# Optimization experiments

Hardware: AMD Instinct MI355X
Metric: run time of the kernel (lower is better)

Reference implementation:

```python
import jax, jax.numpy as jnp
import numpy as np

BITS = 8
BOUND = 2.0 ** (BITS - 1) - 1.0  # 127, symmetric int8 bound
EPS = 1e-6


def fake_quant(x, scale):
    """Symmetric fake quantization with straight-through estimator."""
    q = jnp.clip(jnp.round(x * scale), -BOUND, BOUND) / scale
    return x + jax.lax.stop_gradient(q - x)


def dense_aqt(x, w, b, mask):
    """AQT-style quantized dense: per-tensor input scale (masked stats),
    per-output-channel weight scale, int8-range fake quant, float GEMM.
    x: [N, Cin], w: [Cin, Cout], b: [Cout], mask: [N, 1]."""
    x_max = jnp.max(jnp.abs(x * mask))                       # masked per-tensor stat
    sx = BOUND / jnp.maximum(x_max, EPS)
    w_max = jnp.max(jnp.abs(w), axis=0, keepdims=True)        # [1, Cout]
    sw = BOUND / jnp.maximum(w_max, EPS)
    xq = fake_quant(x, sx)
    wq = fake_quant(w, sw)
    return jnp.matmul(xq, wq) + b


def setup_inputs() -> dict:
    key = jax.random.key(0)
    k1, k2, k3 = jax.random.split(key, 3)
    B, S, C, H = 4, 2048, 1024, 4096
    inputs = jax.random.normal(k1, (B, S, C), dtype=jnp.float32)
    padding_mask = jnp.ones((B, S, 1), dtype=jnp.float32)
    W1 = jax.random.normal(k2, (C, H), dtype=jnp.float32) * (1.0 / np.sqrt(C))
    b1 = jnp.zeros((H,), dtype=jnp.float32)
    W2 = jax.random.normal(k3, (H, C), dtype=jnp.float32) * (1.0 / np.sqrt(H))
    b2 = jnp.zeros((C,), dtype=jnp.float32)
    return {"inputs": inputs, "padding_mask": padding_mask,
            "W1": W1, "b1": b1, "W2": W2, "b2": b2}


def reference(inputs, padding_mask, W1, b1, W2, b2):
    B, S, C = inputs.shape
    x = inputs.reshape(B * S, C)
    m = padding_mask.reshape(B * S, 1)
    h = jax.nn.relu(dense_aqt(x, W1, b1, m))   # dropout is no-op (deterministic)
    out = dense_aqt(h, W2, b2, m)              # dropout is no-op (deterministic)
    return out.reshape(B, S, C)
```

## Files before the change

kernel.cpp:

```cpp
#include <hip/hip_runtime.h>
#include <hip/hip_fp16.h>
#include <stdint.h>


#define EPSQ 1e-6f
typedef int v4i __attribute__((ext_vector_type(4)));
typedef int v16i __attribute__((ext_vector_type(16)));

__device__ __forceinline__ void async16(const int8_t* g, int8_t* l) {
  __builtin_amdgcn_global_load_lds(
      (const __attribute__((address_space(1))) void*)g,
      (__attribute__((address_space(3))) void*)l, 16, 0, 0);
}
__device__ __forceinline__ unsigned short f2h(float f) {
  __half h = __float2half(f);
  return *(unsigned short*)&h;
}
__device__ __forceinline__ float4 max4(float4 m, float4 v) {
  m.x = fmaxf(m.x, fabsf(v.x)); m.y = fmaxf(m.y, fabsf(v.y));
  m.z = fmaxf(m.z, fabsf(v.z)); m.w = fmaxf(m.w, fabsf(v.w));
  return m;
}
__device__ __forceinline__ unsigned qmb(float x, float s) {
  return __float_as_uint(fmaf(x, s, 12582912.0f)) & 0xffu;
}
__device__ __forceinline__ unsigned q4f(float4 f, float s) {
  return qmb(f.x, s) | (qmb(f.y, s) << 8) | (qmb(f.z, s) << 16) |
         (__float_as_uint(fmaf(f.w, s, 12582912.0f)) << 24);
}
__device__ __forceinline__ unsigned q4h(unsigned ua, unsigned ub,
                                        __half2 s2, __half2 m2) {
  __half2 ha = __hfma2(*(__half2*)&ua, s2, m2);
  __half2 hb = __hfma2(*(__half2*)&ub, s2, m2);
  unsigned va = *(unsigned*)&ha, vb = *(unsigned*)&hb;
#if __has_builtin(__builtin_amdgcn_perm)
  return __builtin_amdgcn_perm(vb, va, 0x06040200u);
#else
  return (va & 0xffu) | ((va >> 8) & 0xff00u) |
         ((vb & 0xffu) << 16) | (((vb >> 8) & 0xff00u) << 16);
#endif
}

__global__ __launch_bounds__(256) void k_stats(
    const float* __restrict__ x, const float* __restrict__ mask,
    const float* __restrict__ W1, const float* __restrict__ W2,
    float* __restrict__ pmaxX, float* __restrict__ pcm1, float* __restrict__ pcm2) {
  const int bx = blockIdx.x, tid = threadIdx.x;
  if (bx < 64) {
    const int sp = bx & 15, cg = bx >> 4;
    const int col = cg * 1024 + tid * 4;
    float4 m = {0.f, 0.f, 0.f, 0.f};
#pragma unroll 8
    for (int r = 0; r < 64; ++r)
      m = max4(m, *(const float4*)(W1 + (size_t)(sp * 64 + r) * 4096 + col));
    *(float4*)(pcm1 + sp * 4096 + col) = m;
  } else if (bx < 128) {
    const int sp = bx - 64;
    const int col = tid * 4;
    float4 m = {0.f, 0.f, 0.f, 0.f};
#pragma unroll 8
    for (int r = 0; r < 64; ++r)
      m = max4(m, *(const float4*)(W2 + (size_t)(sp * 64 + r) * 1024 + col));
    *(float4*)(pcm2 + sp * 1024 + col) = m;
  } else {
    __shared__ float red[4];
    const int b = bx - 128;
    float lmax = 0.f;
    for (int c = b * 256 + tid; c < 1048576; c += 262144) {
      size_t idx = (size_t)c * 8;
      float mk = fabsf(mask[idx >> 10]);
      float4 m4 = {0.f, 0.f, 0.f, 0.f};
      m4 = max4(m4, *(const float4*)(x + idx));
      m4 = max4(m4, *(const float4*)(x + idx + 4));
      lmax = fmaxf(lmax, fmaxf(fmaxf(m4.x, m4.y), fmaxf(m4.z, m4.w)) * mk);
    }
    for (int s = 32; s; s >>= 1) lmax = fmaxf(lmax, __shfl_down(lmax, s));
    if ((tid & 63) == 0) red[tid >> 6] = lmax;
    __syncthreads();
    if (tid == 0)
      pmaxX[b] = fmaxf(fmaxf(red[0], red[1]), fmaxf(red[2], red[3]));
  }
}

__global__ __launch_bounds__(256) void k_quant(
    const float* __restrict__ x, const float* __restrict__ W1, const float* __restrict__ W2,
    const float* __restrict__ pmaxX, const float* __restrict__ pcm1, const float* __restrict__ pcm2,
    int8_t* __restrict__ qx, int8_t* __restrict__ qw1, int8_t* __restrict__ qw2,
    float* __restrict__ cm1, float* __restrict__ cm2, float* __restrict__ scG) {
  const int bx = blockIdx.x, tid = threadIdx.x;
  if (bx < 2048) {
    __shared__ float red[4];
    float v = fmaxf(fmaxf(pmaxX[tid], pmaxX[tid + 256]),
                    fmaxf(pmaxX[tid + 512], pmaxX[tid + 768]));
    for (int s = 32; s; s >>= 1) v = fmaxf(v, __shfl_down(v, s));
    if ((tid & 63) == 0) red[tid >> 6] = v;
    __syncthreads();
    const float xmax = fmaxf(fmaxf(red[0], red[1]), fmaxf(red[2], red[3]));
    if (bx == 0 && tid == 0) scG[0] = xmax;
    const float s = 127.0f / fmaxf(xmax, EPSQ);
    const int wave = tid >> 6, lane = tid & 63;
    const int f = bx * 4 + wave;
    const int r = (f >> 5) * 32 + (lane & 31);
    const int k = (f & 31) * 32 + (lane >> 5) * 16;
    const float4* src = (const float4*)(x + (size_t)r * 1024 + k);
    uint4 o;
    o.x = q4f(src[0], s); o.y = q4f(src[1], s);
    o.z = q4f(src[2], s); o.w = q4f(src[3], s);
    *(uint4*)(qx + (size_t)f * 1024 + lane * 16) = o;
  } else if (bx < 2304) {
    int id = (bx - 2048) * 256 + tid;
    int n4 = id & 1023, kc = id >> 10;
    const int col = n4 * 4;
    float4 cm = {0.f, 0.f, 0.f, 0.f};
#pragma unroll
    for (int sp = 0; sp < 16; ++sp) {
      float4 p = *(const float4*)(pcm1 + sp * 4096 + col);
      cm.x = fmaxf(cm.x, p.x); cm.y = fmaxf(cm.y, p.y);
      cm.z = fmaxf(cm.z, p.z); cm.w = fmaxf(cm.w, p.w);
    }
    if (kc == 0) *(float4*)(cm1 + col) = cm;
    const float s0 = 127.0f / fmaxf(cm.x, EPSQ), s1 = 127.0f / fmaxf(cm.y, EPSQ);
    const float s2 = 127.0f / fmaxf(cm.z, EPSQ), s3 = 127.0f / fmaxf(cm.w, EPSQ);
    union { int8_t p[16]; uint4 v; } u0, u1, u2, u3;
#pragma unroll
    for (int j = 0; j < 16; ++j) {
      float4 f = *(const float4*)(W1 + (size_t)(kc * 16 + j) * 4096 + col);
      u0.p[j] = (int8_t)qmb(f.x, s0); u1.p[j] = (int8_t)qmb(f.y, s1);
      u2.p[j] = (int8_t)qmb(f.z, s2); u3.p[j] = (int8_t)qmb(f.w, s3);
    }
    int8_t* base = qw1 + ((size_t)(col >> 5) * 32 + (kc >> 1)) * 1024 +
                   (kc & 1) * 512 + (col & 31) * 16;
    *(uint4*)(base) = u0.v;      *(uint4*)(base + 16) = u1.v;
    *(uint4*)(base + 32) = u2.v; *(uint4*)(base + 48) = u3.v;
  } else {
    int id = (bx - 2304) * 256 + tid;
    int n4 = id & 255, kc = id >> 8;
    const int col = n4 * 4;
    float4 cm = {0.f, 0.f, 0.f, 0.f};
#pragma unroll
    for (int sp = 0; sp < 64; ++sp) {
      float4 p = *(const float4*)(pcm2 + sp * 1024 + col);
      cm.x = fmaxf(cm.x, p.x); cm.y = fmaxf(cm.y, p.y);
      cm.z = fmaxf(cm.z, p.z); cm.w = fmaxf(cm.w, p.w);
    }
    if (kc == 0) *(float4*)(cm2 + col) = cm;
    const float s0 = 127.0f / fmaxf(cm.x, EPSQ), s1 = 127.0f / fmaxf(cm.y, EPSQ);
    const float s2 = 127.0f / fmaxf(cm.z, EPSQ), s3 = 127.0f / fmaxf(cm.w, EPSQ);
    union { int8_t p[16]; uint4 v; } u0, u1, u2, u3;
#pragma unroll
    for (int j = 0; j < 16; ++j) {
      float4 f = *(const float4*)(W2 + (size_t)(kc * 16 + j) * 1024 + col);
      u0.p[j] = (int8_t)qmb(f.x, s0); u1.p[j] = (int8_t)qmb(f.y, s1);
      u2.p[j] = (int8_t)qmb(f.z, s2); u3.p[j] = (int8_t)qmb(f.w, s3);
    }
    int8_t* base = qw2 + ((size_t)(col >> 5) * 128 + (kc >> 1)) * 1024 +
                   (kc & 1) * 512 + (col & 31) * 16;
    *(uint4*)(base) = u0.v;      *(uint4*)(base + 16) = u1.v;
    *(uint4*)(base + 32) = u2.v; *(uint4*)(base + 48) = u3.v;
  }
}

__global__ __launch_bounds__(256, 5) void gemm1(
    const int8_t* __restrict__ A, const int8_t* __restrict__ Bt,
    const float* __restrict__ sxp, const float* __restrict__ cmax,
    const float* __restrict__ bias, const float* __restrict__ mask,
    unsigned short* __restrict__ hfrag, float* __restrict__ pmaxH) {
  constexpr int KF = 2, Kf = 32;
  __shared__ __align__(16) int8_t lsA[2][KF * 4096];
  __shared__ __align__(16) int8_t lsB[2][KF * 4096];
  __shared__ float red[4];
  const int tid = threadIdx.x;
  const int wave = tid >> 6, lane = tid & 63;
  const int m0 = blockIdx.x * 128, n0 = blockIdx.y * 128;
  const int wm = (wave & 1) * 64, wn = (wave >> 1) * 64;

  v16i acc[2][2] = {};

  const int8_t* gA[KF]; const int8_t* gB[KF];
  int8_t* dA[KF]; int8_t* dB[KF];
#pragma unroll
  for (int kc = 0; kc < KF; ++kc) {
    gA[kc] = A + ((size_t)((m0 >> 5) + wave) * Kf + kc) * 1024 + lane * 16;
    gB[kc] = Bt + ((size_t)((n0 >> 5) + wave) * Kf + kc) * 1024 + lane * 16;
    dA[kc] = lsA[0] + (kc * 4 + wave) * 1024 + lane * 16;
    dB[kc] = lsB[0] + (kc * 4 + wave) * 1024 + lane * 16;
  }

  const int nsteps = 1024 / (32 * KF);
#pragma unroll
  for (int kc = 0; kc < KF; ++kc) { async16(gA[kc], dA[kc]); async16(gB[kc], dB[kc]); }

  const int mI = (wave & 1) * 2, nI = (wave >> 1) * 2;

  for (int kb = 0; kb < nsteps; ++kb) {
    const int cur = kb & 1;
    const int co = cur * (KF * 4096);
    __syncthreads();
    if (kb + 1 < nsteps) {
      const size_t ko = (size_t)(kb + 1) * (KF * 1024);
      const int po = (cur ^ 1) * (KF * 4096);
#pragma unroll
      for (int kc = 0; kc < KF; ++kc) {
        async16(gA[kc] + ko, dA[kc] + po);
        async16(gB[kc] + ko, dB[kc] + po);
      }
    }
#pragma unroll
    for (int kc = 0; kc < KF; ++kc) {
      v4i af[2], bf[2];
#pragma unroll
      for (int mt = 0; mt < 2; ++mt)
        af[mt] = *(const v4i*)(lsA[0] + co + (kc * 4 + mI + mt) * 1024 + lane * 16);
#pragma unroll
      for (int nt = 0; nt < 2; ++nt)
        bf[nt] = *(const v4i*)(lsB[0] + co + (kc * 4 + nI + nt) * 1024 + lane * 16);
#pragma unroll
      for (int mt = 0; mt < 2; ++mt)
#pragma unroll
        for (int nt = 0; nt < 2; ++nt)
          acc[mt][nt] = __builtin_amdgcn_mfma_i32_32x32x32_i8(af[mt], bf[nt], acc[mt][nt], 0, 0, 0);
    }
  }

  const float asc = fmaxf(sxp[0], EPSQ) * (1.0f / 127.0f);
  const int cl = lane & 31;
  const int rbase = 4 * (lane >> 5);

  float bsc[2], bv[2];
#pragma unroll
  for (int nt = 0; nt < 2; ++nt) {
    int col = n0 + wn + nt * 32 + cl;
    bsc[nt] = fmaxf(cmax[col], EPSQ) * (1.0f / 127.0f) * asc;
    bv[nt] = bias[col];
  }

  const int hwoff = (cl >> 4) * 512 + (cl & 15);
  float lmax = 0.f;
#pragma unroll
  for (int mt = 0; mt < 2; ++mt) {
    const size_t rowblk = (size_t)((m0 + wm) >> 5) + mt;
#pragma unroll
    for (int g = 0; g < 4; ++g)
#pragma unroll
      for (int r2 = 0; r2 < 4; ++r2) {
        const int rloc = g * 8 + r2 + rbase;
        const int row = m0 + wm + mt * 32 + rloc;
        const float mk = fabsf(mask[row]);
#pragma unroll
        for (int nt = 0; nt < 2; ++nt) {
          const size_t kblk = (size_t)((n0 + wn) >> 5) + nt;
          float v = (float)acc[mt][nt][g * 4 + r2] * bsc[nt] + bv[nt];
          v = fmaxf(v, 0.f);
          hfrag[(rowblk * 128 + kblk) * 1024 + hwoff + rloc * 16] = f2h(v);
          lmax = fmaxf(lmax, v * mk);
        }
      }
  }
  for (int s = 32; s; s >>= 1) lmax = fmaxf(lmax, __shfl_down(lmax, s));
  if (lane == 0) red[wave] = lmax;
  __syncthreads();
  if (tid == 0)
    pmaxH[blockIdx.x * gridDim.y + blockIdx.y] =
        fmaxf(fmaxf(red[0], red[1]), fmaxf(red[2], red[3]));
}

__global__ __launch_bounds__(256, 2) void gemm2(
    const unsigned short* __restrict__ hfrag, const int8_t* __restrict__ Bt,
    const float* __restrict__ pmaxH, const float* __restrict__ cmax,
    const float* __restrict__ bias, float* __restrict__ out) {
  constexpr int KF = 4, Kf = 128;
  __shared__ __align__(16) int8_t lsA[2][KF * 4096];
  __shared__ __align__(16) int8_t lsB[2][KF * 4096];
  __shared__ float red[4];
  const int tid = threadIdx.x;
  const int wave = tid >> 6, lane = tid & 63;

  float v = 0.f;
#pragma unroll
  for (int j = 0; j < 8; ++j) v = fmaxf(v, pmaxH[tid + 256 * j]);
  for (int s = 32; s; s >>= 1) v = fmaxf(v, __shfl_down(v, s));
  if (lane == 0) red[wave] = v;
  __syncthreads();
  const float hmax = fmaxf(fmaxf(red[0], red[1]), fmaxf(red[2], red[3]));
  const float asc = fmaxf(hmax, EPSQ) * (1.0f / 127.0f);
  const __half sh = __float2half_rn(127.0f / fmaxf(hmax, EPSQ));
  const __half2 s2 = __halves2half2(sh, sh);
  const __half mh = __float2half_rn(1536.0f);
  const __half2 m2 = __halves2half2(mh, mh);

  const int m0 = blockIdx.x * 128, n0 = blockIdx.y * 128;
  const int wm = (wave & 1) * 64, wn = (wave >> 1) * 64;

  v16i acc[2][2] = {};

  const uint4* hA = (const uint4*)hfrag;
  size_t aIdx[KF]; const int8_t* gB[KF]; int8_t* dA[KF]; int8_t* dB[KF];
#pragma unroll
  for (int kc = 0; kc < KF; ++kc) {
    aIdx[kc] = ((size_t)((m0 >> 5) + wave) * Kf + kc) * 128 + lane * 2;
    gB[kc] = Bt + ((size_t)((n0 >> 5) + wave) * Kf + kc) * 1024 + lane * 16;
    dA[kc] = lsA[0] + (kc * 4 + wave) * 1024 + lane * 16;
    dB[kc] = lsB[0] + (kc * 4 + wave) * 1024 + lane * 16;
  }

  const int nsteps = 4096 / (32 * KF);
#pragma unroll
  for (int kc = 0; kc < KF; ++kc) {
    uint4 a = hA[aIdx[kc]], b = hA[aIdx[kc] + 1];
    uint4 o;
    o.x = q4h(a.x, a.y, s2, m2); o.y = q4h(a.z, a.w, s2, m2);
    o.z = q4h(b.x, b.y, s2, m2); o.w = q4h(b.z, b.w, s2, m2);
    *(uint4*)dA[kc] = o;
    async16(gB[kc], dB[kc]);
  }

  const int mI = (wave & 1) * 2, nI = (wave >> 1) * 2;

  for (int kb = 0; kb < nsteps; ++kb) {
    const int cur = kb & 1;
    const int co = cur * (KF * 4096);
    __syncthreads();
    uint4 pa[KF], pb[KF];
    const bool more = (kb + 1 < nsteps);
    const int po = (cur ^ 1) * (KF * 4096);
    if (more) {
#pragma unroll
      for (int kc = 0; kc < KF; ++kc) {
        const size_t ai = aIdx[kc] + (size_t)(kb + 1) * (KF * 128);
        pa[kc] = hA[ai];
        pb[kc] = hA[ai + 1];
        async16(gB[kc] + (size_t)(kb + 1) * (KF * 1024), dB[kc] + po);
      }
    }
#pragma unroll
    for (int kc = 0; kc < KF; ++kc) {
      v4i af[2], bf[2];
#pragma unroll
      for (int mt = 0; mt < 2; ++mt)
        af[mt] = *(const v4i*)(lsA[0] + co + (kc * 4 + mI + mt) * 1024 + lane * 16);
#pragma unroll
      for (int nt = 0; nt < 2; ++nt)
        bf[nt] = *(const v4i*)(lsB[0] + co + (kc * 4 + nI + nt) * 1024 + lane * 16);
#pragma unroll
      for (int mt = 0; mt < 2; ++mt)
#pragma unroll
        for (int nt = 0; nt < 2; ++nt)
          acc[mt][nt] = __builtin_amdgcn_mfma_i32_32x32x32_i8(af[mt], bf[nt], acc[mt][nt], 0, 0, 0);
    }
    if (more) {
#pragma unroll
      for (int kc = 0; kc < KF; ++kc) {
        uint4 o;
        o.x = q4h(pa[kc].x, pa[kc].y, s2, m2); o.y = q4h(pa[kc].z, pa[kc].w, s2, m2);
        o.z = q4h(pb[kc].x, pb[kc].y, s2, m2); o.w = q4h(pb[kc].z, pb[kc].w, s2, m2);
        *(uint4*)(dA[kc] + po) = o;
      }
    }
  }

  const int cl = lane & 31;
  const int rbase = 4 * (lane >> 5);
  float bsc[2], bv[2];
#pragma unroll
  for (int nt = 0; nt < 2; ++nt) {
    int col = n0 + wn + nt * 32 + cl;
    bsc[nt] = fmaxf(cmax[col], EPSQ) * (1.0f / 127.0f) * asc;
    bv[nt] = bias[col];
  }
#pragma unroll
  for (int mt = 0; mt < 2; ++mt)
#pragma unroll
    for (int g = 0; g < 4; ++g)
#pragma unroll
      for (int r2 = 0; r2 < 4; ++r2) {
        int row = m0 + wm + mt * 32 + g * 8 + r2 + rbase;
        float* orow = out + (size_t)row * 1024 + n0 + wn + cl;
#pragma unroll
        for (int nt = 0; nt < 2; ++nt)
          orow[nt * 32] = (float)acc[mt][nt][g * 4 + r2] * bsc[nt] + bv[nt];
      }
}

extern "C" void kernel_launch(void* const* d_in, const int* in_sizes, int n_in,
                              void* d_out, int out_size, void* d_ws, size_t ws_size,
                              hipStream_t stream) {
  const float* x  = (const float*)d_in[0];
  const float* mk = (const float*)d_in[1];
  const float* W1 = (const float*)d_in[2];
  const float* b1 = (const float*)d_in[3];
  const float* W2 = (const float*)d_in[4];
  const float* b2 = (const float*)d_in[5];
  float* out = (float*)d_out;

  float* scG   = (float*)d_ws;
  float* pmaxX = scG + 8;
  float* pmaxH = pmaxX + 1024;
  float* pcm1  = pmaxH + 2048;
  float* pcm2  = pcm1 + 65536;
  float* cm1   = pcm2 + 65536;
  float* cm2   = cm1 + 4096;
  int8_t* qx  = (int8_t*)(cm2 + 1024);
  int8_t* qw1 = qx  + (size_t)8192 * 1024;
  int8_t* qw2 = qw1 + (size_t)4096 * 1024;
  unsigned short* h = (unsigned short*)(qw2 + (size_t)1024 * 4096);

  k_stats<<<1152, 256, 0, stream>>>(x, mk, W1, W2, pmaxX, pcm1, pcm2);
  k_quant<<<2560, 256, 0, stream>>>(x, W1, W2, pmaxX, pcm1, pcm2,
                                    qx, qw1, qw2, cm1, cm2, scG);
  gemm1<<<dim3(64, 32), 256, 0, stream>>>(qx, qw1, scG, cm1, b1, mk, h, pmaxH);
  gemm2<<<dim3(64, 8), 256, 0, stream>>>(h, qw2, pmaxH, cm2, b2, out);
}
```

Measured before the change: 237.1 us.

## Stage gemm1 output through swizzled LDS; restructure gemm2 to 8 waves with deeper prefetch

gemm1 now writes its fp16 h fragments into a bank-swizzled LDS tile and then copies them to global memory as coalesced 16-byte stores, replacing scattered 2-byte global writes. gemm2 moves to 512-thread blocks with 8 waves, each computing a 64x32 sub-tile with K-fragment 2. It prefetches the A operand two steps ahead in registers and uses explicit waitcnt/barrier control. It also remaps blocks to XCDs so each XCD handles contiguous M rows for L2 reuse. The risks are more register pressure, extra LDS sync in the gemm1 epilogue, and hand-written waitcnt counts that may be fragile.

```diff
diff --git a/kernel.cpp b/kernel.cpp
--- a/kernel.cpp
+++ b/kernel.cpp
@@ -39,6 +39,9 @@
   return (va & 0xffu) | ((va >> 8) & 0xff00u) |
          ((vb & 0xffu) << 16) | (((vb >> 8) & 0xff00u) << 16);
 #endif
+}
+__device__ __forceinline__ int swzh(int b) {
+  return b ^ (((b >> 10) & 1) << 5) ^ (((b >> 7) & 1) << 6);
 }
 
 __global__ __launch_bounds__(256) void k_stats(
@@ -166,9 +169,9 @@
     const float* __restrict__ bias, const float* __restrict__ mask,
     unsigned short* __restrict__ hfrag, float* __restrict__ pmaxH) {
   constexpr int KF = 2, Kf = 32;
-  __shared__ __align__(16) int8_t lsA[2][KF * 4096];
-  __shared__ __align__(16) int8_t lsB[2][KF * 4096];
-  __shared__ float red[4];
+  __shared__ __align__(16) int8_t smem[32768];
+  int8_t* const lsA = smem;
+  int8_t* const lsB = smem + 16384;
   const int tid = threadIdx.x;
   const int wave = tid >> 6, lane = tid & 63;
   const int m0 = blockIdx.x * 128, n0 = blockIdx.y * 128;
@@ -182,8 +185,8 @@
   for (int kc = 0; kc < KF; ++kc) {
     gA[kc] = A + ((size_t)((m0 >> 5) + wave) * Kf + kc) * 1024 + lane * 16;
     gB[kc] = Bt + ((size_t)((n0 >> 5) + wave) * Kf + kc) * 1024 + lane * 16;
-    dA[kc] = lsA[0] + (kc * 4 + wave) * 1024 + lane * 16;
-    dB[kc] = lsB[0] + (kc * 4 + wave) * 1024 + lane * 16;
+    dA[kc] = lsA + (kc * 4 + wave) * 1024 + lane * 16;
+    dB[kc] = lsB + (kc * 4 + wave) * 1024 + lane * 16;
   }
 
   const int nsteps = 1024 / (32 * KF);
@@ -210,10 +213,10 @@
       v4i af[2], bf[2];
 #pragma unroll
       for (int mt = 0; mt < 2; ++mt)
-        af[mt] = *(const v4i*)(lsA[0] + co + (kc * 4 + mI + mt) * 1024 + lane * 16);
+        af[mt] = *(const v4i*)(lsA + co + (kc * 4 + mI + mt) * 1024 + lane * 16);
 #pragma unroll
       for (int nt = 0; nt < 2; ++nt)
-        bf[nt] = *(const v4i*)(lsB[0] + co + (kc * 4 + nI + nt) * 1024 + lane * 16);
+        bf[nt] = *(const v4i*)(lsB + co + (kc * 4 + nI + nt) * 1024 + lane * 16);
 #pragma unroll
       for (int mt = 0; mt < 2; ++mt)
 #pragma unroll
@@ -234,150 +237,164 @@
     bv[nt] = bias[col];
   }
 
-  const int hwoff = (cl >> 4) * 512 + (cl & 15);
+  const int hwb = ((cl >> 4) * 512 + (cl & 15)) * 2;
   float lmax = 0.f;
+  __syncthreads();
 #pragma unroll
   for (int mt = 0; mt < 2; ++mt) {
-    const size_t rowblk = (size_t)((m0 + wm) >> 5) + mt;
+    const int rbl = (wm >> 5) + mt;
 #pragma unroll
     for (int g = 0; g < 4; ++g)
 #pragma unroll
       for (int r2 = 0; r2 < 4; ++r2) {
         const int rloc = g * 8 + r2 + rbase;
-        const int row = m0 + wm + mt * 32 + rloc;
-        const float mk = fabsf(mask[row]);
+        const float mk = fabsf(mask[m0 + wm + mt * 32 + rloc]);
 #pragma unroll
         for (int nt = 0; nt < 2; ++nt) {
-          const size_t kblk = (size_t)((n0 + wn) >> 5) + nt;
+          const int kbl = (wn >> 5) + nt;
           float v = (float)acc[mt][nt][g * 4 + r2] * bsc[nt] + bv[nt];
           v = fmaxf(v, 0.f);
-          hfrag[(rowblk * 128 + kblk) * 1024 + hwoff + rloc * 16] = f2h(v);
+          *(unsigned short*)(smem + swzh((rbl * 4 + kbl) * 2048 + hwb + rloc * 32)) = f2h(v);
           lmax = fmaxf(lmax, v * mk);
         }
       }
   }
   for (int s = 32; s; s >>= 1) lmax = fmaxf(lmax, __shfl_down(lmax, s));
-  if (lane == 0) red[wave] = lmax;
+  __syncthreads();
+  const size_t gfb = (size_t)(m0 >> 5) * 128 + (n0 >> 5);
+#pragma unroll
+  for (int i = 0; i < 8; ++i) {
+    const int o = i * 4096 + tid * 16;
+    uint4 vv = *(const uint4*)(smem + swzh(o));
+    const int f = o >> 11;
+    *(uint4*)((int8_t*)hfrag +
+              (gfb + (size_t)(f >> 2) * 128 + (f & 3)) * 2048 + (o & 2047)) = vv;
+  }
+  __syncthreads();
+  float* redf = (float*)smem;
+  if (lane == 0) redf[wave] = lmax;
   __syncthreads();
   if (tid == 0)
     pmaxH[blockIdx.x * gridDim.y + blockIdx.y] =
-        fmaxf(fmaxf(red[0], red[1]), fmaxf(red[2], red[3]));
-}
-
-__global__ __launch_bounds__(256, 2) void gemm2(
+        fmaxf(fmaxf(redf[0], redf[1]), fmaxf(redf[2], redf[3]));
+}
+
+__global__ __launch_bounds__(512, 4) void gemm2(
     const unsigned short* __restrict__ hfrag, const int8_t* __restrict__ Bt,
     const float* __restrict__ pmaxH, const float* __restrict__ cmax,
     const float* __restrict__ bias, float* __restrict__ out) {
-  constexpr int KF = 4, Kf = 128;
-  __shared__ __align__(16) int8_t lsA[2][KF * 4096];
-  __shared__ __align__(16) int8_t lsB[2][KF * 4096];
-  __shared__ float red[4];
+  constexpr int KF = 2, Kf = 128;
+  __shared__ __align__(16) int8_t smem[32768];
+  int8_t* const lsA = smem;
+  int8_t* const lsB = smem + 16384;
   const int tid = threadIdx.x;
   const int wave = tid >> 6, lane = tid & 63;
 
+  float* red = (float*)smem;
   float v = 0.f;
 #pragma unroll
-  for (int j = 0; j < 8; ++j) v = fmaxf(v, pmaxH[tid + 256 * j]);
+  for (int j = 0; j < 4; ++j) v = fmaxf(v, pmaxH[tid + 512 * j]);
   for (int s = 32; s; s >>= 1) v = fmaxf(v, __shfl_down(v, s));
   if (lane == 0) red[wave] = v;
   __syncthreads();
-  const float hmax = fmaxf(fmaxf(red[0], red[1]), fmaxf(red[2], red[3]));
+  float hmax = red[0];
+#pragma unroll
+  for (int j = 1; j < 8; ++j) hmax = fmaxf(hmax, red[j]);
+  __syncthreads();
   const float asc = fmaxf(hmax, EPSQ) * (1.0f / 127.0f);
   const __half sh = __float2half_rn(127.0f / fmaxf(hmax, EPSQ));
   const __half2 s2 = __halves2half2(sh, sh);
   const __half mh = __float2half_rn(1536.0f);
   const __half2 m2 = __halves2half2(mh, mh);
 
-  const int m0 = blockIdx.x * 128, n0 = blockIdx.y * 128;
-  const int wm = (wave & 1) * 64, wn = (wave >> 1) * 64;
-
-  v16i acc[2][2] = {};
-
+  const int bid = blockIdx.x;
+  const int xcd = bid & 7, slot = bid >> 3;
+  const int m0 = ((xcd << 3) + (slot >> 3)) * 128;
+  const int n0 = (slot & 7) * 128;
+  const int wm = (wave & 1) * 64, wn = (wave >> 1) * 32;
+
+  v16i acc[2] = {};
+
+  const int skc = wave >> 2, sfr = wave & 3;
   const uint4* hA = (const uint4*)hfrag;
-  size_t aIdx[KF]; const int8_t* gB[KF]; int8_t* dA[KF]; int8_t* dB[KF];
-#pragma unroll
-  for (int kc = 0; kc < KF; ++kc) {
-    aIdx[kc] = ((size_t)((m0 >> 5) + wave) * Kf + kc) * 128 + lane * 2;
-    gB[kc] = Bt + ((size_t)((n0 >> 5) + wave) * Kf + kc) * 1024 + lane * 16;
-    dA[kc] = lsA[0] + (kc * 4 + wave) * 1024 + lane * 16;
-    dB[kc] = lsB[0] + (kc * 4 + wave) * 1024 + lane * 16;
-  }
+  const size_t aIdx = ((size_t)((m0 >> 5) + sfr) * Kf + skc) * 128 + lane * 2;
+  const int8_t* gB = Bt + ((size_t)((n0 >> 5) + sfr) * Kf + skc) * 1024 + lane * 16;
+  int8_t* const dA = lsA + (skc * 4 + sfr) * 1024 + lane * 16;
+  int8_t* const dB = lsB + (skc * 4 + sfr) * 1024 + lane * 16;
 
   const int nsteps = 4096 / (32 * KF);
-#pragma unroll
-  for (int kc = 0; kc < KF; ++kc) {
-    uint4 a = hA[aIdx[kc]], b = hA[aIdx[kc] + 1];
+  const int mI = (wave & 1) * 2, nb = wave >> 1;
+
+  uint4 rA0 = {0, 0, 0, 0}, rB0 = {0, 0, 0, 0};
+  uint4 rA1 = {0, 0, 0, 0}, rB1 = {0, 0, 0, 0};
+
+  {
+    uint4 a = hA[aIdx], b = hA[aIdx + 1];
+    async16(gB, dB);
+    __builtin_amdgcn_sched_barrier(0);
+    rA1 = hA[aIdx + (size_t)(KF * 128)];
+    rB1 = hA[aIdx + (size_t)(KF * 128) + 1];
     uint4 o;
     o.x = q4h(a.x, a.y, s2, m2); o.y = q4h(a.z, a.w, s2, m2);
     o.z = q4h(b.x, b.y, s2, m2); o.w = q4h(b.z, b.w, s2, m2);
-    *(uint4*)dA[kc] = o;
-    async16(gB[kc], dB[kc]);
-  }
-
-  const int mI = (wave & 1) * 2, nI = (wave >> 1) * 2;
-
+    *(uint4*)dA = o;
+  }
+  asm volatile("s_waitcnt lgkmcnt(0)" ::: "memory");
+  asm volatile("s_waitcnt vmcnt(2)" ::: "memory");
+  __builtin_amdgcn_s_barrier();
+  __builtin_amdgcn_sched_barrier(0);
+
+#pragma unroll 2
   for (int kb = 0; kb < nsteps; ++kb) {
     const int cur = kb & 1;
-    const int co = cur * (KF * 4096);
-    __syncthreads();
-    uint4 pa[KF], pb[KF];
+    const int co = cur * 8192, po = co ^ 8192;
     const bool more = (kb + 1 < nsteps);
-    const int po = (cur ^ 1) * (KF * 4096);
+    const bool deep = (kb + 2 < nsteps);
     if (more) {
-#pragma unroll
-      for (int kc = 0; kc < KF; ++kc) {
-        const size_t ai = aIdx[kc] + (size_t)(kb + 1) * (KF * 128);
-        pa[kc] = hA[ai];
-        pb[kc] = hA[ai + 1];
-        async16(gB[kc] + (size_t)(kb + 1) * (KF * 1024), dB[kc] + po);
+      async16(gB + (size_t)(kb + 1) * (KF * 1024), dB + po);
+      __builtin_amdgcn_sched_barrier(0);
+      if (deep) {
+        const size_t ai = aIdx + (size_t)(kb + 2) * (KF * 128);
+        if (cur) { rA1 = hA[ai]; rB1 = hA[ai + 1]; }
+        else     { rA0 = hA[ai]; rB0 = hA[ai + 1]; }
       }
     }
 #pragma unroll
     for (int kc = 0; kc < KF; ++kc) {
-      v4i af[2], bf[2];
-#pragma unroll
-      for (int mt = 0; mt < 2; ++mt)
-        af[mt] = *(const v4i*)(lsA[0] + co + (kc * 4 + mI + mt) * 1024 + lane * 16);
-#pragma unroll
-      for (int nt = 0; nt < 2; ++nt)
-        bf[nt] = *(const v4i*)(lsB[0] + co + (kc * 4 + nI + nt) * 1024 + lane * 16);
-#pragma unroll
-      for (int mt = 0; mt < 2; ++mt)
-#pragma unroll
-        for (int nt = 0; nt < 2; ++nt)
-          acc[mt][nt] = __builtin_amdgcn_mfma_i32_32x32x32_i8(af[mt], bf[nt], acc[mt][nt], 0, 0, 0);
+      v4i af0 = *(const v4i*)(lsA + co + (kc * 4 + mI) * 1024 + lane * 16);
+      v4i af1 = *(const v4i*)(lsA + co + (kc * 4 + mI + 1) * 1024 + lane * 16);
+      v4i bf  = *(const v4i*)(lsB + co + (kc * 4 + nb) * 1024 + lane * 16);
+      acc[0] = __builtin_amdgcn_mfma_i32_32x32x32_i8(af0, bf, acc[0], 0, 0, 0);
+      acc[1] = __builtin_amdgcn_mfma_i32_32x32x32_i8(af1, bf, acc[1], 0, 0, 0);
     }
     if (more) {
-#pragma unroll
-      for (int kc = 0; kc < KF; ++kc) {
-        uint4 o;
-        o.x = q4h(pa[kc].x, pa[kc].y, s2, m2); o.y = q4h(pa[kc].z, pa[kc].w, s2, m2);
-        o.z = q4h(pb[kc].x, pb[kc].y, s2, m2); o.w = q4h(pb[kc].z, pb[kc].w, s2, m2);
-        *(uint4*)(dA[kc] + po) = o;
-      }
+      const uint4 pa = cur ? rA0 : rA1;
+      const uint4 pb = cur ? rB0 : rB1;
+      uint4 o;
+      o.x = q4h(pa.x, pa.y, s2, m2); o.y = q4h(pa.z, pa.w, s2, m2);
+      o.z = q4h(pb.x, pb.y, s2, m2); o.w = q4h(pb.z, pb.w, s2, m2);
+      *(uint4*)(dA + po) = o;
+      asm volatile("s_waitcnt lgkmcnt(0)" ::: "memory");
+      if (deep) asm volatile("s_waitcnt vmcnt(2)" ::: "memory");
+      else      asm volatile("s_waitcnt vmcnt(0)" ::: "memory");
+      __builtin_amdgcn_s_barrier();
+      __builtin_amdgcn_sched_barrier(0);
     }
   }
 
   const int cl = lane & 31;
   const int rbase = 4 * (lane >> 5);
-  float bsc[2], bv[2];
-#pragma unroll
-  for (int nt = 0; nt < 2; ++nt) {
-    int col = n0 + wn + nt * 32 + cl;
-    bsc[nt] = fmaxf(cmax[col], EPSQ) * (1.0f / 127.0f) * asc;
-    bv[nt] = bias[col];
-  }
+  const int col = n0 + wn + cl;
+  const float bsc = fmaxf(cmax[col], EPSQ) * (1.0f / 127.0f) * asc;
+  const float bv = bias[col];
 #pragma unroll
   for (int mt = 0; mt < 2; ++mt)
 #pragma unroll
     for (int g = 0; g < 4; ++g)
 #pragma unroll
       for (int r2 = 0; r2 < 4; ++r2) {
-        int row = m0 + wm + mt * 32 + g * 8 + r2 + rbase;
-        float* orow = out + (size_t)row * 1024 + n0 + wn + cl;
-#pragma unroll
-        for (int nt = 0; nt < 2; ++nt)
-          orow[nt * 32] = (float)acc[mt][nt][g * 4 + r2] * bsc[nt] + bv[nt];
+        const int row = m0 + wm + mt * 32 + g * 8 + r2 + rbase;
+        out[(size_t)row * 1024 + col] = (float)acc[mt][g * 4 + r2] * bsc + bv;
       }
 }
 
@@ -408,5 +425,5 @@
   k_quant<<<2560, 256, 0, stream>>>(x, W1, W2, pmaxX, pcm1, pcm2,
                                     qx, qw1, qw2, cm1, cm2, scG);
   gemm1<<<dim3(64, 32), 256, 0, stream>>>(qx, qw1, scG, cm1, b1, mk, h, pmaxH);
-  gemm2<<<dim3(64, 8), 256, 0, stream>>>(h, qw2, pmaxH, cm2, b2, out);
-}
+  gemm2<<<512, 512, 0, stream>>>(h, qw2, pmaxH, cm2, b2, out);
+}
```

Result: slower. 243.4 us (+2.6%).
